# Performance work log

Hardware: AMD Instinct MI355X
Metric: run time of the kernel (lower is better)

Reference implementation:

```python
import jax, jax.numpy as jnp
import numpy as np
import math

SIZE = 1024

def fwht(x):
    # Fast Walsh-Hadamard transform over the last axis (size must be power of 2).
    orig_shape = x.shape
    size = orig_shape[-1]
    x = x.reshape(-1, size)
    h = 1
    while h < size:
        # blocks of 2h: index = b*(2h) + k*h + j, k in {0,1}
        xr = x.reshape(-1, size // (2 * h), 2, h)
        u = xr[:, :, 0, :]
        v = xr[:, :, 1, :]
        x = jnp.stack([u + v, u - v], axis=2).reshape(-1, size)
        h *= 2
    return x.reshape(orig_shape)

def setup_inputs() -> dict:
    key = jax.random.key(0)
    kx, = jax.random.split(key, 1)
    x = jax.random.normal(kx, (8, 8192, SIZE), dtype=jnp.float32)
    scale = jnp.ones((SIZE,), dtype=jnp.float32)
    shift = jnp.zeros((SIZE,), dtype=jnp.float32)
    return {"x": x, "scale": scale, "shift": shift}

def reference(x, scale, shift):
    size = x.shape[-1]
    xt = fwht(x) * (1.0 / math.sqrt(size))  # normalize=True
    return scale * xt + shift
```

## Files before the change

### kernel.cpp

```cpp
#include <hip/hip_runtime.h>


constexpr int SIZE = 1024;
constexpr float INV_SQRT = 0.03125f;

__global__ __launch_bounds__(256) void fwht1024_kernel(
    const float* __restrict__ x,
    const float* __restrict__ scale,
    const float* __restrict__ shift,
    float* __restrict__ out,
    int nrows)
{
    const int wave = threadIdx.x >> 6;
    const int lane = threadIdx.x & 63;
    const int row  = blockIdx.x * 4 + wave;
    if (row >= nrows) return;

    const float* __restrict__ xr = x + (size_t)row * SIZE;
    float* __restrict__ orow     = out + (size_t)row * SIZE;

    float v[4][4];
    #pragma unroll
    for (int j = 0; j < 4; ++j) {
        const float4 t = *reinterpret_cast<const float4*>(xr + 256 * j + 4 * lane);
        v[j][0] = t.x; v[j][1] = t.y; v[j][2] = t.z; v[j][3] = t.w;
    }

    #pragma unroll
    for (int j = 0; j < 4; ++j) {
        const float a = v[j][0], b = v[j][1], c = v[j][2], d = v[j][3];
        const float ab = a + b, amb = a - b, cd = c + d, cmd = c - d;
        v[j][0] = ab + cd; v[j][1] = amb + cmd;
        v[j][2] = ab - cd; v[j][3] = amb - cmd;
    }

    #pragma unroll
    for (int m = 1; m <= 32; m <<= 1) {
        const bool upper = (lane & m) != 0;
        #pragma unroll
        for (int j = 0; j < 4; ++j) {
            #pragma unroll
            for (int r = 0; r < 4; ++r) {
                const float o = __shfl_xor(v[j][r], m, 64);
                v[j][r] = upper ? (o - v[j][r]) : (v[j][r] + o);
            }
        }
    }

    #pragma unroll
    for (int r = 0; r < 4; ++r) {
        const float a = v[0][r], b = v[1][r], c = v[2][r], d = v[3][r];
        const float ab = a + b, amb = a - b, cd = c + d, cmd = c - d;
        v[0][r] = ab + cd; v[1][r] = amb + cmd;
        v[2][r] = ab - cd; v[3][r] = amb - cmd;
    }

    #pragma unroll
    for (int j = 0; j < 4; ++j) {
        const int base = 256 * j + 4 * lane;
        const float4 sc = *reinterpret_cast<const float4*>(scale + base);
        const float4 sh = *reinterpret_cast<const float4*>(shift + base);
        float4 o;
        o.x = fmaf(v[j][0] * INV_SQRT, sc.x, sh.x);
        o.y = fmaf(v[j][1] * INV_SQRT, sc.y, sh.y);
        o.z = fmaf(v[j][2] * INV_SQRT, sc.z, sh.z);
        o.w = fmaf(v[j][3] * INV_SQRT, sc.w, sh.w);
        *reinterpret_cast<float4*>(orow + base) = o;
    }
}

extern "C" void kernel_launch(void* const* d_in, const int* in_sizes, int n_in,
                              void* d_out, int out_size, void* d_ws, size_t ws_size,
                              hipStream_t stream)
{
    const float* x     = (const float*)d_in[0];
    const float* scale = (const float*)d_in[1];
    const float* shift = (const float*)d_in[2];
    float* out         = (float*)d_out;

    const int nrows = in_sizes[0] / SIZE;
    const int blocks = (nrows + 3) / 4;

    fwht1024_kernel<<<blocks, 256, 0, stream>>>(x, scale, shift, out, nrows);
}
```

Measured before the change: 425.6 us.

## Replace cross-lane shuffles with padded LDS transposes for FWHT butterflies

Removes the six rounds of 16 cross-lane shuffles. The butterfly stages are regrouped so lanes swap data through a padded per-wave shared-memory buffer: two transposes, then in-register radix-16 butterflies. The final output is written with scalar nontemporal stores, and scale/shift are read as scalars. This trades shuffle latency and instruction count for LDS traffic and narrower global stores, which could hurt a memory-bound kernel.

```diff
diff --git a/kernel.cpp b/kernel.cpp
--- a/kernel.cpp
+++ b/kernel.cpp
@@ -11,13 +11,15 @@
     float* __restrict__ out,
     int nrows)
 {
+    __shared__ float lds[4][1300];
+
     const int wave = threadIdx.x >> 6;
     const int lane = threadIdx.x & 63;
     const int row  = blockIdx.x * 4 + wave;
     if (row >= nrows) return;
 
+    float* __restrict__ sm = lds[wave];
     const float* __restrict__ xr = x + (size_t)row * SIZE;
-    float* __restrict__ orow     = out + (size_t)row * SIZE;
 
     float v[4][4];
     #pragma unroll
@@ -33,18 +35,26 @@
         v[j][0] = ab + cd; v[j][1] = amb + cmd;
         v[j][2] = ab - cd; v[j][3] = amb - cmd;
     }
+    #pragma unroll
+    for (int r = 0; r < 4; ++r) {
+        const float a = v[0][r], b = v[1][r], c = v[2][r], d = v[3][r];
+        const float ab = a + b, amb = a - b, cd = c + d, cmd = c - d;
+        v[0][r] = ab + cd; v[1][r] = amb + cmd;
+        v[2][r] = ab - cd; v[3][r] = amb - cmd;
+    }
 
+    const int wbase = 20 * (lane >> 2) + 4 * (lane & 3);
     #pragma unroll
-    for (int m = 1; m <= 32; m <<= 1) {
-        const bool upper = (lane & m) != 0;
-        #pragma unroll
-        for (int j = 0; j < 4; ++j) {
-            #pragma unroll
-            for (int r = 0; r < 4; ++r) {
-                const float o = __shfl_xor(v[j][r], m, 64);
-                v[j][r] = upper ? (o - v[j][r]) : (v[j][r] + o);
-            }
-        }
+    for (int j = 0; j < 4; ++j) {
+        float4 t; t.x = v[j][0]; t.y = v[j][1]; t.z = v[j][2]; t.w = v[j][3];
+        *reinterpret_cast<float4*>(sm + 328 * j + wbase) = t;
+    }
+
+    const int rbase = 20 * lane + 8 * (lane >> 4);
+    #pragma unroll
+    for (int k = 0; k < 4; ++k) {
+        const float4 t = *reinterpret_cast<const float4*>(sm + rbase + 4 * k);
+        v[k][0] = t.x; v[k][1] = t.y; v[k][2] = t.z; v[k][3] = t.w;
     }
 
     #pragma unroll
@@ -56,16 +66,36 @@
     }
 
     #pragma unroll
-    for (int j = 0; j < 4; ++j) {
-        const int base = 256 * j + 4 * lane;
-        const float4 sc = *reinterpret_cast<const float4*>(scale + base);
-        const float4 sh = *reinterpret_cast<const float4*>(shift + base);
-        float4 o;
-        o.x = fmaf(v[j][0] * INV_SQRT, sc.x, sh.x);
-        o.y = fmaf(v[j][1] * INV_SQRT, sc.y, sh.y);
-        o.z = fmaf(v[j][2] * INV_SQRT, sc.z, sh.z);
-        o.w = fmaf(v[j][3] * INV_SQRT, sc.w, sh.w);
-        *reinterpret_cast<float4*>(orow + base) = o;
+    for (int k = 0; k < 4; ++k) {
+        float4 t; t.x = v[k][0]; t.y = v[k][1]; t.z = v[k][2]; t.w = v[k][3];
+        *reinterpret_cast<float4*>(sm + rbase + 4 * k) = t;
+    }
+
+    const int base3 = 328 * (lane >> 4) + (lane & 15);
+    float w[16];
+    #pragma unroll
+    for (int r16 = 0; r16 < 16; ++r16)
+        w[r16] = sm[base3 + 20 * r16];
+
+    #pragma unroll
+    for (int m = 1; m <= 8; m <<= 1) {
+        #pragma unroll
+        for (int p = 0; p < 16; ++p) {
+            if (!(p & m)) {
+                const float u = w[p], t = w[p | m];
+                w[p] = u + t; w[p | m] = u - t;
+            }
+        }
+    }
+
+    const int ebase = ((lane >> 4) << 8) + (lane & 15);
+    float* __restrict__ orow = out + (size_t)row * SIZE;
+    #pragma unroll
+    for (int r16 = 0; r16 < 16; ++r16) {
+        const int e = ebase + 16 * r16;
+        const float sc = scale[e];
+        const float sh = shift[e];
+        __builtin_nontemporal_store(fmaf(w[r16] * INV_SQRT, sc, sh), orow + e);
     }
 }
 
```

Measured after the change: 437.3 us. 2.8% more time.
